# Kernel optimization log

Measured on AMD Instinct MI355X. Metric: run time of the kernel, lower is better.

The kernel has to match this reference:

```python
import jax, jax.numpy as jnp
import numpy as np

DIM = 2048
HEADS = 16
DIM_HEAD = 128
FF_MULT = 4
FF_INNER = DIM * FF_MULT  # 8192
ATTN_INNER = HEADS * DIM_HEAD  # 2048
FUSED_OUT = ATTN_INNER + DIM_HEAD + DIM_HEAD + 2 * FF_INNER
LN_EPS = 1e-5


def setup_inputs() -> dict:
    key = jax.random.key(0)
    k1, k2, k3, k4, k5 = jax.random.split(key, 5)
    b, n = 2, 2048
    x = jax.random.normal(k1, (b, n, DIM), dtype=jnp.float32)
    vl = jax.random.randint(k2, (b,), 1, n + 1)  # valid lengths in [1, n]
    gamma = jnp.ones((DIM,), dtype=jnp.float32)
    w_fused = jax.random.normal(k3, (DIM, FUSED_OUT), dtype=jnp.float32) * 0.02
    w_attn_out = jax.random.normal(k4, (ATTN_INNER, DIM), dtype=jnp.float32) * 0.02
    w_ff_out = jax.random.normal(k5, (FF_INNER, DIM), dtype=jnp.float32) * 0.02
    return {"x": x, "vl": vl, "gamma": gamma, "w_fused": w_fused,
            "w_attn_out": w_attn_out, "w_ff_out": w_ff_out}


def _rotate_half(t):
    t1, t2 = jnp.split(t, 2, axis=-1)
    return jnp.concatenate((-t2, t1), axis=-1)


def _apply_rope(pos, t):
    return t * jnp.cos(pos) + _rotate_half(t) * jnp.sin(pos)


def reference(x, vl, gamma, w_fused, w_attn_out, w_ff_out):
    b, n, _ = x.shape
    # LayerNorm (learned gamma, beta = 0)
    mu = jnp.mean(x, axis=-1, keepdims=True)
    var = jnp.mean(jnp.square(x - mu), axis=-1, keepdims=True)
    xn = (x - mu) * jax.lax.rsqrt(var + LN_EPS) * gamma
    # fused QKV + FF projection
    fused = xn @ w_fused  # [b, n, FUSED_OUT]
    q = fused[..., :ATTN_INNER]
    k = fused[..., ATTN_INNER:ATTN_INNER + DIM_HEAD]
    v = fused[..., ATTN_INNER + DIM_HEAD:ATTN_INNER + 2 * DIM_HEAD]
    ff = fused[..., ATTN_INNER + 2 * DIM_HEAD:]
    q = q.reshape(b, n, HEADS, DIM_HEAD).transpose(0, 2, 1, 3)  # b h n d
    # rotary embedding: half-split convention, cat(freqs, freqs)
    inv_freq = 1.0 / (10000.0 ** (jnp.arange(0, DIM_HEAD, 2, dtype=jnp.float32) / DIM_HEAD))
    freqs = jnp.arange(n, dtype=jnp.float32)[:, None] * inv_freq[None, :]  # [n, d/2]
    pos = jnp.concatenate((freqs, freqs), axis=-1)  # [n, d]
    q = _apply_rope(pos, q)
    k = _apply_rope(pos, k)  # k: [b, n, d] (MQA single head)
    q = q * (DIM_HEAD ** -0.5)
    sim = jnp.einsum('bhid,bjd->bhij', q, k)
    # key padding mask: True where position >= valid length (invalid keys)
    pad = jnp.arange(n)[None, :] >= vl[:, None]  # [b, n]
    sim = jnp.where(pad[:, None, None, :], -jnp.inf, sim)
    attn = jax.nn.softmax(sim, axis=-1)
    out = jnp.einsum('bhij,bjd->bhid', attn, v)
    out = out.transpose(0, 2, 1, 3).reshape(b, n, ATTN_INNER)
    attn_out = out @ w_attn_out
    # SwiGLU: chunk(2) -> (x_part, gate); silu(gate) * x_part
    ff_x, ff_gate = jnp.split(ff, 2, axis=-1)
    ff_out = (jax.nn.silu(ff_gate) * ff_x) @ w_ff_out
    return attn_out + ff_out
```

## Files before the change

kernel.cpp:

```cpp
#include <hip/hip_runtime.h>
#include <hip/hip_bf16.h>

typedef __hip_bfloat16 bf16;
typedef __attribute__((ext_vector_type(4))) float f32x4;
typedef __attribute__((ext_vector_type(8))) short short8;

#define DEV __device__ __forceinline__
#define MFMA16(a, b, c) __builtin_amdgcn_mfma_f32_16x16x32_bf16(a, b, c, 0, 0, 0)

DEV void gload16(const void* g, void* l) {
  __builtin_amdgcn_global_load_lds((const __attribute__((address_space(1))) void*)g,
                                   (__attribute__((address_space(3))) void*)l, 16, 0, 0);
}

DEV unsigned short f2b(float f) {
  return __builtin_bit_cast(unsigned short, __float2bfloat16(f));
}

#define S_BARRIER() asm volatile("s_barrier" ::: "memory")
#define LGKM0()                                              \
  do {                                                       \
    asm volatile("s_waitcnt lgkmcnt(0)" ::: "memory");       \
    __builtin_amdgcn_sched_barrier(0);                       \
  } while (0)

__global__ __launch_bounds__(256) void transpose_cast_kernel(
    const float* __restrict__ src, bf16* __restrict__ dst, int R, int C, int permff)
{
  __shared__ float tile[32][33];
  const int c0 = blockIdx.x * 32, k0 = blockIdx.y * 32;
  const int tx = threadIdx.x, ty = threadIdx.y;
#pragma unroll
  for (int r = 0; r < 4; ++r)
    tile[ty + 8 * r][tx] = src[(size_t)(k0 + ty + 8 * r) * C + c0 + tx];
  __syncthreads();
#pragma unroll
  for (int r = 0; r < 4; ++r) {
    int c = c0 + ty + 8 * r;
    int n = c;
    if (permff && c >= 2304) {
      int f = c - 2304;
      if (f < 8192) n = 2304 + ((f >> 4) << 5) + (f & 15);
      else { int f2 = f - 8192; n = 2304 + ((f2 >> 4) << 5) + 16 + (f2 & 15); }
    }
    dst[(size_t)n * R + k0 + tx] = __float2bfloat16(tile[tx][ty + 8 * r]);
  }
}

__global__ __launch_bounds__(256) void ln_kernel(
    const float* __restrict__ x, const float* __restrict__ gamma, bf16* __restrict__ o)
{
  const int row = blockIdx.x;
  const int t = threadIdx.x;
  const float4* xv = (const float4*)(x + (size_t)row * 2048) + t * 2;
  float4 a = xv[0], b = xv[1];
  float v[8] = {a.x, a.y, a.z, a.w, b.x, b.y, b.z, b.w};
  float s = 0.f, sq = 0.f;
#pragma unroll
  for (int i = 0; i < 8; ++i) { s += v[i]; sq += v[i] * v[i]; }
#pragma unroll
  for (int off = 32; off >= 1; off >>= 1) {
    s += __shfl_xor(s, off);
    sq += __shfl_xor(sq, off);
  }
  __shared__ float red[8];
  const int wave = t >> 6, lane = t & 63;
  if (lane == 0) { red[wave] = s; red[4 + wave] = sq; }
  __syncthreads();
  s = red[0] + red[1] + red[2] + red[3];
  sq = red[4] + red[5] + red[6] + red[7];
  const float mu = s * (1.f / 2048.f);
  const float var = sq * (1.f / 2048.f) - mu * mu;
  const float rs = rsqrtf(var + 1e-5f);
  const float4* gv = (const float4*)gamma + t * 2;
  float4 g0 = gv[0], g1 = gv[1];
  float gg[8] = {g0.x, g0.y, g0.z, g0.w, g1.x, g1.y, g1.z, g1.w};
  short8 pk;
#pragma unroll
  for (int i = 0; i < 8; ++i) pk[i] = f2b((v[i] - mu) * rs * gg[i]);
  *(short8*)(o + (size_t)row * 2048 + t * 8) = pk;
}

template <int MODE, int WN>
__global__ __launch_bounds__(512, 2) void gemm8p(
    const bf16* __restrict__ A, const bf16* __restrict__ Bw,
    int Kd, int NT_M,
    bf16* __restrict__ oq, bf16* __restrict__ okk, bf16* __restrict__ ovt,
    bf16* __restrict__ og, float* __restrict__ of)
{
  constexpr int MR = (WN == 4) ? 8 : 4;
  constexpr int BN = WN * 64;
  constexpr int ABYTES = 32768;
  constexpr int BBYTES = BN * 64 * 2;
  constexpr int BUFB = ABYTES + BBYTES;
  constexpr int VW = 2 + (WN >> 1);
  __shared__ __align__(16) char ldsb[2 * BUFB];

  const int t = threadIdx.x;
  const int lane = t & 63, wid = t >> 6;
  const int il = lane & 15, kg = lane >> 4;
  const int wn = wid % WN, wm = wid / WN;

  const int nwg = gridDim.x;
  const int bid = blockIdx.x;
  const int v = (bid & 7) * (nwg >> 3) + (bid >> 3);
  const int tm = v % NT_M, tn = v / NT_M;

  const int l16 = lane * 16;
  const int w0 = l16 ^ (((l16 >> 9) & 1) << 5);
  const int r_in = w0 >> 6;
  const int c_in = (w0 & 63) >> 1;

  const int swz = (il * 64 + kg * 16) ^ ((il >> 3) << 5);

  const bf16* Abase = A + (size_t)(tm * 256) * Kd;
  const bf16* Bbase = Bw + (size_t)(tn * BN) * Kd;
  const size_t laneOff = (size_t)r_in * Kd + c_in;

  const int NT = Kd >> 6;

  f32x4 acc[MR][4];
#pragma unroll
  for (int m = 0; m < MR; ++m)
#pragma unroll
    for (int n = 0; n < 4; ++n) acc[m][n] = (f32x4){0.f, 0.f, 0.f, 0.f};

  auto stageA = [&](int b, int k0, int kh) {
#pragma unroll
    for (int s = 0; s < 2; ++s) {
      const int sr = wid * 2 + s;
      gload16(Abase + (size_t)(sr * 16) * Kd + (k0 + kh * 32) + laneOff,
              ldsb + b * BUFB + (sr * 2 + kh) * 1024 + l16);
    }
  };
  auto stageB = [&](int b, int k0, int kh) {
    if constexpr (WN == 4) {
#pragma unroll
      for (int s = 0; s < 2; ++s) {
        const int sr = wid * 2 + s;
        gload16(Bbase + (size_t)(sr * 16) * Kd + (k0 + kh * 32) + laneOff,
                ldsb + b * BUFB + ABYTES + (sr * 2 + kh) * 1024 + l16);
      }
    } else {
      const int sr = wid;
      gload16(Bbase + (size_t)(sr * 16) * Kd + (k0 + kh * 32) + laneOff,
              ldsb + b * BUFB + ABYTES + (sr * 2 + kh) * 1024 + l16);
    }
  };
  auto rdA = [&](int b, int m, int ks) -> short8 {
    return *(const short8*)(ldsb + b * BUFB + (wm * MR + m) * 2048 + ks * 1024 + swz);
  };
  auto rdB = [&](int b, int n, int ks) -> short8 {
    return *(const short8*)(ldsb + b * BUFB + ABYTES + (wn * 4 + n) * 2048 + ks * 1024 + swz);
  };

  stageA(0, 0, 0);
  stageB(0, 0, 0);
  stageA(0, 0, 1);
  stageB(0, 0, 1);
  asm volatile("s_waitcnt vmcnt(%0)" ::"n"(VW) : "memory");
  S_BARRIER();

  short8 a0[MR], a1[MR], b0[4], b1[4];

  for (int jt = 0; jt < NT; ++jt) {
    const int b = jt & 1, nb = b ^ 1;
    const int k1 = (jt + 1) << 6;
    const bool hn = (jt + 1) < NT;

#pragma unroll
    for (int m = 0; m < MR; ++m) a0[m] = rdA(b, m, 0);
    b0[0] = rdB(b, 0, 0);
    b0[1] = rdB(b, 1, 0);
    if (hn) stageA(nb, k1, 0);
    S_BARRIER();
    LGKM0();
    __builtin_amdgcn_s_setprio(1);
#pragma unroll
    for (int m = 0; m < MR; ++m) {
      acc[m][0] = MFMA16(a0[m], b0[0], acc[m][0]);
      acc[m][1] = MFMA16(a0[m], b0[1], acc[m][1]);
    }
    __builtin_amdgcn_s_setprio(0);
    S_BARRIER();

    b0[2] = rdB(b, 2, 0);
    b0[3] = rdB(b, 3, 0);
    if (hn) stageB(nb, k1, 0);
    S_BARRIER();
    LGKM0();
    __builtin_amdgcn_s_setprio(1);
#pragma unroll
    for (int m = 0; m < MR; ++m) {
      acc[m][2] = MFMA16(a0[m], b0[2], acc[m][2]);
      acc[m][3] = MFMA16(a0[m], b0[3], acc[m][3]);
    }
    __builtin_amdgcn_s_setprio(0);
    if (hn) { asm volatile("s_waitcnt vmcnt(%0)" ::"n"(VW) : "memory"); }
    else    { asm volatile("s_waitcnt vmcnt(0)" ::: "memory"); }
    S_BARRIER();

#pragma unroll
    for (int m = 0; m < MR; ++m) a1[m] = rdA(b, m, 1);
    b1[0] = rdB(b, 0, 1);
    b1[1] = rdB(b, 1, 1);
    if (hn) stageA(nb, k1, 1);
    S_BARRIER();
    LGKM0();
    __builtin_amdgcn_s_setprio(1);
#pragma unroll
    for (int m = 0; m < MR; ++m) {
      acc[m][0] = MFMA16(a1[m], b1[0], acc[m][0]);
      acc[m][1] = MFMA16(a1[m], b1[1], acc[m][1]);
    }
    __builtin_amdgcn_s_setprio(0);
    S_BARRIER();

    b1[2] = rdB(b, 2, 1);
    b1[3] = rdB(b, 3, 1);
    if (hn) stageB(nb, k1, 1);
    S_BARRIER();
    LGKM0();
    __builtin_amdgcn_s_setprio(1);
#pragma unroll
    for (int m = 0; m < MR; ++m) {
      acc[m][2] = MFMA16(a1[m], b1[2], acc[m][2]);
      acc[m][3] = MFMA16(a1[m], b1[3], acc[m][3]);
    }
    __builtin_amdgcn_s_setprio(0);
    if (hn) { asm volatile("s_waitcnt vmcnt(%0)" ::"n"(VW) : "memory"); }
    S_BARRIER();
  }

  const int rb = tm * 256 + wm * (WN * 32);
  const int cb = tn * BN + wn * 64;

  if constexpr (MODE == 0) {
    if (cb < 2048) {
#pragma unroll
      for (int m = 0; m < MR; ++m)
#pragma unroll
        for (int n = 0; n < 4; ++n)
#pragma unroll
          for (int r = 0; r < 4; ++r)
            oq[(size_t)(rb + m * 16 + kg * 4 + r) * 2048 + cb + n * 16 + il] =
                __float2bfloat16(acc[m][n][r]);
    } else if (cb < 2176) {
#pragma unroll
      for (int m = 0; m < MR; ++m)
#pragma unroll
        for (int n = 0; n < 4; ++n)
#pragma unroll
          for (int r = 0; r < 4; ++r)
            okk[(size_t)(rb + m * 16 + kg * 4 + r) * 128 + (cb - 2048 + n * 16 + il)] =
                __float2bfloat16(acc[m][n][r]);
    } else if (cb < 2304) {
#pragma unroll
      for (int m = 0; m < MR; ++m)
#pragma unroll
        for (int n = 0; n < 4; ++n)
#pragma unroll
          for (int r = 0; r < 4; ++r) {
            int R = rb + m * 16 + kg * 4 + r;
            int d = cb - 2176 + n * 16 + il;
            ovt[(size_t)(R >> 11) * (128 * 2048) + (size_t)d * 2048 + (R & 2047)] =
                __float2bfloat16(acc[m][n][r]);
          }
    } else {
#pragma unroll
      for (int m = 0; m < MR; ++m)
#pragma unroll
        for (int n = 0; n < 4; n += 2) {
          int p0 = ((cb + n * 16 - 2304) >> 5) * 16 + il;
#pragma unroll
          for (int r = 0; r < 4; ++r) {
            float xv = acc[m][n][r];
            float gvv = acc[m][n + 1][r];
            float ga = xv * gvv / (1.f + __expf(-gvv));
            og[(size_t)(rb + m * 16 + kg * 4 + r) * 8192 + p0] = __float2bfloat16(ga);
          }
        }
    }
  } else {
#pragma unroll
    for (int m = 0; m < MR; ++m)
#pragma unroll
      for (int n = 0; n < 4; ++n)
#pragma unroll
        for (int r = 0; r < 4; ++r) {
          size_t idx = (size_t)(rb + m * 16 + kg * 4 + r) * 2048 + cb + n * 16 + il;
          if constexpr (MODE == 1) of[idx] = acc[m][n][r];
          else of[idx] += acc[m][n][r];
        }
  }
}

__global__ __launch_bounds__(256) void rope_q_kernel(bf16* __restrict__ q)
{
  const int idx = blockIdx.x * 256 + threadIdx.x;
  const int d = idx & 63;
  const int h = (idx >> 6) & 15;
  const int i = (idx >> 10) & 2047;
  const int b = idx >> 21;
  const size_t base = ((size_t)(b * 2048 + i)) * 2048 + h * 128 + d;
  const float x1 = __bfloat162float(q[base]);
  const float x2 = __bfloat162float(q[base + 64]);
  const double inv = exp2(-0.20762050593045972 * (double)d);
  const float ang = (float)((double)i * inv);
  const float sn = sinf(ang), cs = cosf(ang);
  const float sc = 0.08838834764831845f;
  q[base] = __float2bfloat16((x1 * cs - x2 * sn) * sc);
  q[base + 64] = __float2bfloat16((x2 * cs + x1 * sn) * sc);
}

__global__ __launch_bounds__(256) void rope_k_kernel(bf16* __restrict__ k)
{
  const int idx = blockIdx.x * 256 + threadIdx.x;
  const int d = idx & 63;
  const int i = (idx >> 6) & 2047;
  const int b = idx >> 17;
  const size_t base = ((size_t)(b * 2048 + i)) * 128 + d;
  const float x1 = __bfloat162float(k[base]);
  const float x2 = __bfloat162float(k[base + 64]);
  const double inv = exp2(-0.20762050593045972 * (double)d);
  const float ang = (float)((double)i * inv);
  const float sn = sinf(ang), cs = cosf(ang);
  k[base] = __float2bfloat16(x1 * cs - x2 * sn);
  k[base + 64] = __float2bfloat16(x2 * cs + x1 * sn);
}

__global__ __launch_bounds__(256) void attn_kernel(
    const bf16* __restrict__ q, const bf16* __restrict__ kb, const bf16* __restrict__ vt,
    bf16* __restrict__ out, const int* __restrict__ vl)
{
  __shared__ __align__(16) unsigned char smem[51200];
  bf16* Ks = (bf16*)smem;
  const int t = threadIdx.x, lane = t & 63, wave = t >> 6;
  const int il = lane & 15, kg = lane >> 4;
  const int bh = blockIdx.y, b = bh >> 4, h = bh & 15;
  const int i0 = blockIdx.x * 64;
  const int vlb = vl[b];
  bf16* Plw = (bf16*)(smem + 32768 + wave * 4608);

  const int qrow = b * 2048 + i0 + wave * 16 + il;
  const bf16* qp = q + (size_t)qrow * 2048 + h * 128 + kg * 8;
  short8 qf[4];
#pragma unroll
  for (int kd = 0; kd < 4; ++kd) qf[kd] = *(const short8*)(qp + kd * 32);

  const bf16* vtb = vt + (size_t)b * (128 * 2048);

  f32x4 ot[8];
#pragma unroll
  for (int i = 0; i < 8; ++i) ot[i] = (f32x4){0.f, 0.f, 0.f, 0.f};
  float mrun = -1e30f, lrun = 0.f;

  const int ntile = (vlb + 127) >> 7;
  for (int tt = 0; tt < ntile; ++tt) {
    const int j0 = tt << 7;
#pragma unroll
    for (int u = 0; u < 8; ++u) {
      int id = u * 256 + t;
      int row = id >> 4, cc = id & 15;
      int csw = cc ^ (row & 7);
      gload16(kb + (size_t)(b * 2048 + j0 + row) * 128 + csw * 8, Ks + id * 8);
    }
    __syncthreads();
    f32x4 st[8];
#pragma unroll
    for (int jb = 0; jb < 8; ++jb) {
      f32x4 a = (f32x4){0.f, 0.f, 0.f, 0.f};
      const int row = jb * 16 + il;
      const int rx = row & 7;
#pragma unroll
      for (int kd = 0; kd < 4; ++kd) {
        int slot = (kd * 4 + kg) ^ rx;
        short8 kf = *(const short8*)(Ks + row * 128 + slot * 8);
        a = MFMA16(kf, qf[kd], a);
      }
      st[jb] = a;
    }
    if (j0 + 128 > vlb) {
#pragma unroll
      for (int jb = 0; jb < 8; ++jb)
#pragma unroll
        for (int r = 0; r < 4; ++r)
          if (j0 + jb * 16 + kg * 4 + r >= vlb) st[jb][r] = -1e30f;
    }
    float tmax = -1e30f;
#pragma unroll
    for (int jb = 0; jb < 8; ++jb)
#pragma unroll
      for (int r = 0; r < 4; ++r) tmax = fmaxf(tmax, st[jb][r]);
    tmax = fmaxf(tmax, __shfl_xor(tmax, 16));
    tmax = fmaxf(tmax, __shfl_xor(tmax, 32));
    const float mnew = fmaxf(mrun, tmax);
    const float scale = __expf(mrun - mnew);
    float ls = 0.f;
#pragma unroll
    for (int jb = 0; jb < 8; ++jb)
#pragma unroll
      for (int r = 0; r < 4; ++r) {
        float p = __expf(st[jb][r] - mnew);
        st[jb][r] = p;
        ls += p;
      }
    ls += __shfl_xor(ls, 16);
    ls += __shfl_xor(ls, 32);
    lrun = lrun * scale + ls;
    mrun = mnew;
#pragma unroll
    for (int db = 0; db < 8; ++db) ot[db] *= scale;
#pragma unroll
    for (int jb = 0; jb < 8; ++jb)
#pragma unroll
      for (int r = 0; r < 4; ++r)
        Plw[il * 144 + jb * 16 + kg * 4 + r] = __float2bfloat16(st[jb][r]);
#pragma unroll
    for (int db = 0; db < 8; ++db) {
      const bf16* vp = vtb + (size_t)(db * 16 + il) * 2048 + j0 + kg * 8;
      f32x4 o = ot[db];
#pragma unroll
      for (int kj = 0; kj < 4; ++kj) {
        short8 vf = *(const short8*)(vp + kj * 32);
        short8 pf = *(const short8*)(Plw + il * 144 + kj * 32 + kg * 8);
        o = MFMA16(vf, pf, o);
      }
      ot[db] = o;
    }
    __syncthreads();
  }

  const float inv = 1.f / lrun;
#pragma unroll
  for (int db = 0; db < 8; ++db) ot[db] *= inv;

  float* Osw = (float*)smem + wave * 2112;
#pragma unroll
  for (int db = 0; db < 8; ++db)
#pragma unroll
    for (int r = 0; r < 4; ++r)
      Osw[il * 132 + db * 16 + kg * 4 + r] = ot[db][r];
  const int orow = lane >> 2;
  const int seg = lane & 3;
  const size_t obase = (size_t)(b * 2048 + i0 + wave * 16 + orow) * 2048 + h * 128 + seg * 32;
#pragma unroll
  for (int u = 0; u < 4; ++u) {
    short8 pk;
#pragma unroll
    for (int e = 0; e < 8; ++e) pk[e] = f2b(Osw[orow * 132 + seg * 32 + u * 8 + e]);
    *(short8*)(out + obase + u * 8) = pk;
  }
}

extern "C" void kernel_launch(void* const* d_in, const int* in_sizes, int n_in,
                              void* d_out, int out_size, void* d_ws, size_t ws_size,
                              hipStream_t stream)
{
  const float* x       = (const float*)d_in[0];
  const int*   vl      = (const int*)d_in[1];
  const float* gamma   = (const float*)d_in[2];
  const float* w_fused = (const float*)d_in[3];
  const float* w_attn  = (const float*)d_in[4];
  const float* w_ff    = (const float*)d_in[5];
  float* out = (float*)d_out;
  char* ws = (char*)d_ws;

  bf16* wfT  = (bf16*)(ws);
  bf16* waoT = (bf16*)(ws + 76546048);
  bf16* wffT = (bf16*)(ws + 84934656);
  bf16* xn   = (bf16*)(ws + 118489088);
  bf16* qb   = (bf16*)(ws + 135266304);
  bf16* kb   = (bf16*)(ws + 152043520);
  bf16* vtb  = (bf16*)(ws + 153092096);
  bf16* gb   = (bf16*)(ws + 154140672);

  transpose_cast_kernel<<<dim3(584, 64), dim3(32, 8), 0, stream>>>(w_fused, wfT, 2048, 18688, 1);
  transpose_cast_kernel<<<dim3(64, 64), dim3(32, 8), 0, stream>>>(w_attn, waoT, 2048, 2048, 0);
  transpose_cast_kernel<<<dim3(64, 256), dim3(32, 8), 0, stream>>>(w_ff, wffT, 8192, 2048, 0);
  ln_kernel<<<4096, 256, 0, stream>>>(x, gamma, xn);
  gemm8p<0, 4><<<dim3(1168), 512, 0, stream>>>(xn, wfT, 2048, 16,
                                               qb, kb, vtb, gb, nullptr);
  rope_q_kernel<<<16384, 256, 0, stream>>>(qb);
  rope_k_kernel<<<1024, 256, 0, stream>>>(kb);
  attn_kernel<<<dim3(32, 32), 256, 0, stream>>>(qb, kb, vtb, qb, vl);
  gemm8p<1, 2><<<dim3(256), 512, 0, stream>>>(qb, waoT, 2048, 16,
                                              nullptr, nullptr, nullptr, nullptr, out);
  gemm8p<2, 2><<<dim3(256), 512, 0, stream>>>(gb, wffT, 8192, 16,
                                              nullptr, nullptr, nullptr, nullptr, out);
}
```

Baseline: 1.070 ms.

## Fuse output GEMMs via K-concatenation, fold Q rope into attention, widen transpose

The attention-output and FF-output GEMMs become one GEMM whose K dimension runs over the attention output and then the gated FF activations. This removes the second launch and the read-modify-write of the fp32 output. Q rotary embedding now happens in registers inside the attention kernel, which drops a separate pass over Q. The weight transpose uses 64x64 tiles with vectorized loads and stores, rope_k uses float exp2 instead of double, and the GEMM main loop reorders its LDS reads, stage issue and vmcnt waits. The exchange is a per-stage source-select branch in the GEMM loader and some precision change in the rope angle computation.

```diff
diff --git a/kernel.cpp b/kernel.cpp
--- a/kernel.cpp
+++ b/kernel.cpp
@@ -16,34 +16,45 @@
 DEV unsigned short f2b(float f) {
   return __builtin_bit_cast(unsigned short, __float2bfloat16(f));
 }
+DEV float b2f(short u) {
+  unsigned int x = ((unsigned int)(unsigned short)u) << 16;
+  return __builtin_bit_cast(float, x);
+}
 
 #define S_BARRIER() asm volatile("s_barrier" ::: "memory")
-#define LGKM0()                                              \
-  do {                                                       \
-    asm volatile("s_waitcnt lgkmcnt(0)" ::: "memory");       \
-    __builtin_amdgcn_sched_barrier(0);                       \
-  } while (0)
-
-__global__ __launch_bounds__(256) void transpose_cast_kernel(
+
+__global__ __launch_bounds__(256) void transpose_cast2(
     const float* __restrict__ src, bf16* __restrict__ dst, int R, int C, int permff)
 {
-  __shared__ float tile[32][33];
-  const int c0 = blockIdx.x * 32, k0 = blockIdx.y * 32;
-  const int tx = threadIdx.x, ty = threadIdx.y;
-#pragma unroll
-  for (int r = 0; r < 4; ++r)
-    tile[ty + 8 * r][tx] = src[(size_t)(k0 + ty + 8 * r) * C + c0 + tx];
+  __shared__ float tile[64][65];
+  const int c0 = blockIdx.x * 64, k0 = blockIdx.y * 64;
+  const int t = threadIdx.x;
+  const int lr = t >> 4;
+  const int lc = (t & 15) * 4;
+#pragma unroll
+  for (int rep = 0; rep < 4; ++rep) {
+    const int r = lr + rep * 16;
+    const float4 vv = *(const float4*)(src + (size_t)(k0 + r) * C + c0 + lc);
+    tile[r][lc] = vv.x; tile[r][lc + 1] = vv.y;
+    tile[r][lc + 2] = vv.z; tile[r][lc + 3] = vv.w;
+  }
   __syncthreads();
-#pragma unroll
-  for (int r = 0; r < 4; ++r) {
-    int c = c0 + ty + 8 * r;
+  const int ln = t >> 3;
+  const int lk = (t & 7) * 8;
+#pragma unroll
+  for (int rep = 0; rep < 2; ++rep) {
+    const int cc = ln + rep * 32;
+    const int c = c0 + cc;
     int n = c;
     if (permff && c >= 2304) {
       int f = c - 2304;
       if (f < 8192) n = 2304 + ((f >> 4) << 5) + (f & 15);
       else { int f2 = f - 8192; n = 2304 + ((f2 >> 4) << 5) + 16 + (f2 & 15); }
     }
-    dst[(size_t)n * R + k0 + tx] = __float2bfloat16(tile[tx][ty + 8 * r]);
+    short8 pk;
+#pragma unroll
+    for (int e = 0; e < 8; ++e) pk[e] = f2b(tile[lk + e][cc]);
+    *(short8*)(dst + (size_t)n * R + k0 + lk) = pk;
   }
 }
 
@@ -83,8 +94,9 @@
 
 template <int MODE, int WN>
 __global__ __launch_bounds__(512, 2) void gemm8p(
-    const bf16* __restrict__ A, const bf16* __restrict__ Bw,
-    int Kd, int NT_M,
+    const bf16* __restrict__ A1, int lda1, const bf16* __restrict__ A2, int lda2,
+    const bf16* __restrict__ B1, int ldb1, const bf16* __restrict__ B2, int ldb2,
+    int ksplit, int Kd, int NT_M,
     bf16* __restrict__ oq, bf16* __restrict__ okk, bf16* __restrict__ ovt,
     bf16* __restrict__ og, float* __restrict__ of)
 {
@@ -93,7 +105,7 @@
   constexpr int ABYTES = 32768;
   constexpr int BBYTES = BN * 64 * 2;
   constexpr int BUFB = ABYTES + BBYTES;
-  constexpr int VW = 2 + (WN >> 1);
+  constexpr int FP4 = (WN == 4) ? 2 : 1;
   __shared__ __align__(16) char ldsb[2 * BUFB];
 
   const int t = threadIdx.x;
@@ -113,10 +125,6 @@
 
   const int swz = (il * 64 + kg * 16) ^ ((il >> 3) << 5);
 
-  const bf16* Abase = A + (size_t)(tm * 256) * Kd;
-  const bf16* Bbase = Bw + (size_t)(tn * BN) * Kd;
-  const size_t laneOff = (size_t)r_in * Kd + c_in;
-
   const int NT = Kd >> 6;
 
   f32x4 acc[MR][4];
@@ -125,56 +133,66 @@
 #pragma unroll
     for (int n = 0; n < 4; ++n) acc[m][n] = (f32x4){0.f, 0.f, 0.f, 0.f};
 
-  auto stageA = [&](int b, int k0, int kh) {
+  auto stageA = [&](int buf, int k0t, int kh) {
+    const bool sec = k0t >= ksplit;
+    const int ld = sec ? lda2 : lda1;
+    const bf16* base = (sec ? A2 : A1) + (size_t)(tm * 256) * ld;
+    const int kk = k0t - (sec ? ksplit : 0) + kh * 32;
+    const size_t lo = (size_t)r_in * ld + c_in + kk;
 #pragma unroll
     for (int s = 0; s < 2; ++s) {
       const int sr = wid * 2 + s;
-      gload16(Abase + (size_t)(sr * 16) * Kd + (k0 + kh * 32) + laneOff,
-              ldsb + b * BUFB + (sr * 2 + kh) * 1024 + l16);
+      gload16(base + (size_t)(sr * 16) * ld + lo,
+              ldsb + buf * BUFB + (sr * 2 + kh) * 1024 + l16);
     }
   };
-  auto stageB = [&](int b, int k0, int kh) {
+  auto stageB = [&](int buf, int k0t, int kh) {
+    const bool sec = k0t >= ksplit;
+    const int ld = sec ? ldb2 : ldb1;
+    const bf16* base = (sec ? B2 : B1) + (size_t)(tn * BN) * ld;
+    const int kk = k0t - (sec ? ksplit : 0) + kh * 32;
+    const size_t lo = (size_t)r_in * ld + c_in + kk;
     if constexpr (WN == 4) {
 #pragma unroll
       for (int s = 0; s < 2; ++s) {
         const int sr = wid * 2 + s;
-        gload16(Bbase + (size_t)(sr * 16) * Kd + (k0 + kh * 32) + laneOff,
-                ldsb + b * BUFB + ABYTES + (sr * 2 + kh) * 1024 + l16);
+        gload16(base + (size_t)(sr * 16) * ld + lo,
+                ldsb + buf * BUFB + ABYTES + (sr * 2 + kh) * 1024 + l16);
       }
     } else {
       const int sr = wid;
-      gload16(Bbase + (size_t)(sr * 16) * Kd + (k0 + kh * 32) + laneOff,
-              ldsb + b * BUFB + ABYTES + (sr * 2 + kh) * 1024 + l16);
+      gload16(base + (size_t)(sr * 16) * ld + lo,
+              ldsb + buf * BUFB + ABYTES + (sr * 2 + kh) * 1024 + l16);
     }
   };
-  auto rdA = [&](int b, int m, int ks) -> short8 {
-    return *(const short8*)(ldsb + b * BUFB + (wm * MR + m) * 2048 + ks * 1024 + swz);
+  auto rdA = [&](int buf, int m, int ks) -> short8 {
+    return *(const short8*)(ldsb + buf * BUFB + (wm * MR + m) * 2048 + ks * 1024 + swz);
   };
-  auto rdB = [&](int b, int n, int ks) -> short8 {
-    return *(const short8*)(ldsb + b * BUFB + ABYTES + (wn * 4 + n) * 2048 + ks * 1024 + swz);
+  auto rdB = [&](int buf, int n, int ks) -> short8 {
+    return *(const short8*)(ldsb + buf * BUFB + ABYTES + (wn * 4 + n) * 2048 + ks * 1024 + swz);
   };
 
   stageA(0, 0, 0);
+  stageA(0, 0, 1);
   stageB(0, 0, 0);
-  stageA(0, 0, 1);
   stageB(0, 0, 1);
-  asm volatile("s_waitcnt vmcnt(%0)" ::"n"(VW) : "memory");
+  asm volatile("s_waitcnt vmcnt(%0)" ::"n"(FP4) : "memory");
   S_BARRIER();
 
   short8 a0[MR], a1[MR], b0[4], b1[4];
 
   for (int jt = 0; jt < NT; ++jt) {
-    const int b = jt & 1, nb = b ^ 1;
+    const int buf = jt & 1, nb = buf ^ 1;
     const int k1 = (jt + 1) << 6;
     const bool hn = (jt + 1) < NT;
 
-#pragma unroll
-    for (int m = 0; m < MR; ++m) a0[m] = rdA(b, m, 0);
-    b0[0] = rdB(b, 0, 0);
-    b0[1] = rdB(b, 1, 0);
+    b0[0] = rdB(buf, 0, 0);
+    b0[1] = rdB(buf, 1, 0);
+#pragma unroll
+    for (int m = 0; m < MR; ++m) a0[m] = rdA(buf, m, 0);
     if (hn) stageA(nb, k1, 0);
     S_BARRIER();
-    LGKM0();
+    __builtin_amdgcn_sched_barrier(0);
     __builtin_amdgcn_s_setprio(1);
 #pragma unroll
     for (int m = 0; m < MR; ++m) {
@@ -182,13 +200,17 @@
       acc[m][1] = MFMA16(a0[m], b0[1], acc[m][1]);
     }
     __builtin_amdgcn_s_setprio(0);
-    S_BARRIER();
-
-    b0[2] = rdB(b, 2, 0);
-    b0[3] = rdB(b, 3, 0);
-    if (hn) stageB(nb, k1, 0);
-    S_BARRIER();
-    LGKM0();
+    if (hn) { asm volatile("s_waitcnt vmcnt(2)" ::: "memory"); }
+    else    { asm volatile("s_waitcnt vmcnt(0)" ::: "memory"); }
+    S_BARRIER();
+
+    b0[2] = rdB(buf, 2, 0);
+    b0[3] = rdB(buf, 3, 0);
+    b1[0] = rdB(buf, 0, 1);
+    b1[1] = rdB(buf, 1, 1);
+    if (hn) stageA(nb, k1, 1);
+    S_BARRIER();
+    __builtin_amdgcn_sched_barrier(0);
     __builtin_amdgcn_s_setprio(1);
 #pragma unroll
     for (int m = 0; m < MR; ++m) {
@@ -196,17 +218,13 @@
       acc[m][3] = MFMA16(a0[m], b0[3], acc[m][3]);
     }
     __builtin_amdgcn_s_setprio(0);
-    if (hn) { asm volatile("s_waitcnt vmcnt(%0)" ::"n"(VW) : "memory"); }
-    else    { asm volatile("s_waitcnt vmcnt(0)" ::: "memory"); }
-    S_BARRIER();
-
-#pragma unroll
-    for (int m = 0; m < MR; ++m) a1[m] = rdA(b, m, 1);
-    b1[0] = rdB(b, 0, 1);
-    b1[1] = rdB(b, 1, 1);
-    if (hn) stageA(nb, k1, 1);
-    S_BARRIER();
-    LGKM0();
+    S_BARRIER();
+
+#pragma unroll
+    for (int m = 0; m < MR; ++m) a1[m] = rdA(buf, m, 1);
+    if (hn) stageB(nb, k1, 0);
+    S_BARRIER();
+    __builtin_amdgcn_sched_barrier(0);
     __builtin_amdgcn_s_setprio(1);
 #pragma unroll
     for (int m = 0; m < MR; ++m) {
@@ -216,11 +234,11 @@
     __builtin_amdgcn_s_setprio(0);
     S_BARRIER();
 
-    b1[2] = rdB(b, 2, 1);
-    b1[3] = rdB(b, 3, 1);
+    b1[2] = rdB(buf, 2, 1);
+    b1[3] = rdB(buf, 3, 1);
     if (hn) stageB(nb, k1, 1);
     S_BARRIER();
-    LGKM0();
+    __builtin_amdgcn_sched_barrier(0);
     __builtin_amdgcn_s_setprio(1);
 #pragma unroll
     for (int m = 0; m < MR; ++m) {
@@ -228,7 +246,8 @@
       acc[m][3] = MFMA16(a1[m], b1[3], acc[m][3]);
     }
     __builtin_amdgcn_s_setprio(0);
-    if (hn) { asm volatile("s_waitcnt vmcnt(%0)" ::"n"(VW) : "memory"); }
+    if (hn) { asm volatile("s_waitcnt vmcnt(%0)" ::"n"(FP4) : "memory"); }
+    else    { asm volatile("s_waitcnt vmcnt(0)" ::: "memory"); }
     S_BARRIER();
   }
 
@@ -287,30 +306,9 @@
 #pragma unroll
       for (int n = 0; n < 4; ++n)
 #pragma unroll
-        for (int r = 0; r < 4; ++r) {
-          size_t idx = (size_t)(rb + m * 16 + kg * 4 + r) * 2048 + cb + n * 16 + il;
-          if constexpr (MODE == 1) of[idx] = acc[m][n][r];
-          else of[idx] += acc[m][n][r];
-        }
-  }
-}
-
-__global__ __launch_bounds__(256) void rope_q_kernel(bf16* __restrict__ q)
-{
-  const int idx = blockIdx.x * 256 + threadIdx.x;
-  const int d = idx & 63;
-  const int h = (idx >> 6) & 15;
-  const int i = (idx >> 10) & 2047;
-  const int b = idx >> 21;
-  const size_t base = ((size_t)(b * 2048 + i)) * 2048 + h * 128 + d;
-  const float x1 = __bfloat162float(q[base]);
-  const float x2 = __bfloat162float(q[base + 64]);
-  const double inv = exp2(-0.20762050593045972 * (double)d);
-  const float ang = (float)((double)i * inv);
-  const float sn = sinf(ang), cs = cosf(ang);
-  const float sc = 0.08838834764831845f;
-  q[base] = __float2bfloat16((x1 * cs - x2 * sn) * sc);
-  q[base + 64] = __float2bfloat16((x2 * cs + x1 * sn) * sc);
+        for (int r = 0; r < 4; ++r)
+          of[(size_t)(rb + m * 16 + kg * 4 + r) * 2048 + cb + n * 16 + il] = acc[m][n][r];
+  }
 }
 
 __global__ __launch_bounds__(256) void rope_k_kernel(bf16* __restrict__ k)
@@ -322,8 +320,8 @@
   const size_t base = ((size_t)(b * 2048 + i)) * 128 + d;
   const float x1 = __bfloat162float(k[base]);
   const float x2 = __bfloat162float(k[base + 64]);
-  const double inv = exp2(-0.20762050593045972 * (double)d);
-  const float ang = (float)((double)i * inv);
+  const float inv = __builtin_exp2f(-0.20762050593045972f * (float)d);
+  const float ang = (float)i * inv;
   const float sn = sinf(ang), cs = cosf(ang);
   k[base] = __float2bfloat16(x1 * cs - x2 * sn);
   k[base + 64] = __float2bfloat16(x2 * cs + x1 * sn);
@@ -348,6 +346,24 @@
 #pragma unroll
   for (int kd = 0; kd < 4; ++kd) qf[kd] = *(const short8*)(qp + kd * 32);
 
+  {
+    const int ipos = i0 + wave * 16 + il;
+    const float sc = 0.08838834764831845f;
+#pragma unroll
+    for (int kd2 = 0; kd2 < 2; ++kd2)
+#pragma unroll
+      for (int e = 0; e < 8; ++e) {
+        const int d = kd2 * 32 + kg * 8 + e;
+        const float inv = __builtin_exp2f(-0.20762050593045972f * (float)d);
+        const float ang = (float)ipos * inv;
+        const float sn = sinf(ang), cs = cosf(ang);
+        const float q0 = b2f(qf[kd2][e]);
+        const float q1 = b2f(qf[kd2 + 2][e]);
+        qf[kd2][e]     = f2b((q0 * cs - q1 * sn) * sc);
+        qf[kd2 + 2][e] = f2b((q1 * cs + q0 * sn) * sc);
+      }
+  }
+
   const bf16* vtb = vt + (size_t)b * (128 * 2048);
 
   f32x4 ot[8];
@@ -475,17 +491,18 @@
   bf16* vtb  = (bf16*)(ws + 153092096);
   bf16* gb   = (bf16*)(ws + 154140672);
 
-  transpose_cast_kernel<<<dim3(584, 64), dim3(32, 8), 0, stream>>>(w_fused, wfT, 2048, 18688, 1);
-  transpose_cast_kernel<<<dim3(64, 64), dim3(32, 8), 0, stream>>>(w_attn, waoT, 2048, 2048, 0);
-  transpose_cast_kernel<<<dim3(64, 256), dim3(32, 8), 0, stream>>>(w_ff, wffT, 8192, 2048, 0);
+  const int KBIG = 1 << 30;
+
+  transpose_cast2<<<dim3(292, 32), 256, 0, stream>>>(w_fused, wfT, 2048, 18688, 1);
+  transpose_cast2<<<dim3(32, 32), 256, 0, stream>>>(w_attn, waoT, 2048, 2048, 0);
+  transpose_cast2<<<dim3(32, 128), 256, 0, stream>>>(w_ff, wffT, 8192, 2048, 0);
   ln_kernel<<<4096, 256, 0, stream>>>(x, gamma, xn);
-  gemm8p<0, 4><<<dim3(1168), 512, 0, stream>>>(xn, wfT, 2048, 16,
-                                               qb, kb, vtb, gb, nullptr);
-  rope_q_kernel<<<16384, 256, 0, stream>>>(qb);
+  gemm8p<0, 4><<<dim3(1168), 512, 0, stream>>>(
+      xn, 2048, xn, 2048, wfT, 2048, wfT, 2048, KBIG, 2048, 16,
+      qb, kb, vtb, gb, nullptr);
   rope_k_kernel<<<1024, 256, 0, stream>>>(kb);
   attn_kernel<<<dim3(32, 32), 256, 0, stream>>>(qb, kb, vtb, qb, vl);
-  gemm8p<1, 2><<<dim3(256), 512, 0, stream>>>(qb, waoT, 2048, 16,
-                                              nullptr, nullptr, nullptr, nullptr, out);
-  gemm8p<2, 2><<<dim3(256), 512, 0, stream>>>(gb, wffT, 8192, 16,
-                                              nullptr, nullptr, nullptr, nullptr, out);
-}
+  gemm8p<1, 2><<<dim3(256), 512, 0, stream>>>(
+      qb, 2048, gb, 8192, waoT, 2048, wffT, 8192, 2048, 10240, 16,
+      nullptr, nullptr, nullptr, nullptr, out);
+}
```

After: 1.086 ms. About the same (+1.5%).
